# Performance work log

Measured on AMD Instinct MI355X. Metric: run time of the kernel, lower is better.

The kernel has to match this reference:

```python
import jax, jax.numpy as jnp
import numpy as np

B, L, D = 2, 2048, 2048
N, K, H = 16, 8, 128
EPS = 1e-6
ROPE_THETA = 1000000
K_MASK = -2.3819763e+38


def rms_norm(x, w, eps=EPS):
    dtype = x.dtype
    rms = jnp.sqrt(jnp.mean(x.astype(jnp.float32) ** 2, axis=-1, keepdims=True) + eps)
    return (w * x / rms).astype(dtype)


def apply_rope(inputs, positions, head_dim, rope_theta=ROPE_THETA):
    # inputs: [B, L, n, H], positions: [B, L]
    fraction = 2 * jnp.arange(0, head_dim // 2, dtype=jnp.float32) / head_dim
    timescale = rope_theta ** fraction  # [H/2]
    sinusoid = positions[..., jnp.newaxis] / timescale[jnp.newaxis, jnp.newaxis, :]  # [B,L,H/2]
    sinusoid = sinusoid[..., jnp.newaxis, :]  # [B,L,1,H/2]
    sin, cos = jnp.sin(sinusoid), jnp.cos(sinusoid)
    first, second = jnp.split(inputs, 2, axis=-1)
    out = jnp.concatenate([first * cos - second * sin, second * cos + first * sin], axis=-1)
    return out.astype(inputs.dtype)


def setup_inputs() -> dict:
    key = jax.random.key(0)
    ks = jax.random.split(key, 6)
    x = jax.random.normal(ks[0], (B, L, D), dtype=jnp.float32)
    position_ids = jnp.broadcast_to(jnp.arange(L, dtype=jnp.int32)[None, :], (B, L))
    # causal mask [B, L, S]
    attn_mask = jnp.broadcast_to(jnp.tril(jnp.ones((L, L), dtype=bool))[None], (B, L, L))
    wq = jax.random.normal(ks[1], (D, N, H), dtype=jnp.float32) * 0.02
    wk = jax.random.normal(ks[2], (D, K, H), dtype=jnp.float32) * 0.02
    wv = jax.random.normal(ks[3], (D, K, H), dtype=jnp.float32) * 0.02
    wo = jax.random.normal(ks[4], (N, H, D), dtype=jnp.float32) * 0.02
    q_norm_w = jnp.ones((H,), dtype=jnp.float32)
    k_norm_w = jnp.ones((H,), dtype=jnp.float32)
    return {"x": x, "position_ids": position_ids, "attn_mask": attn_mask,
            "wq": wq, "wk": wk, "wv": wv, "wo": wo,
            "q_norm_w": q_norm_w, "k_norm_w": k_norm_w}


def reference(x, position_ids, attn_mask, wq, wk, wv, wo, q_norm_w, k_norm_w):
    scale = H ** (-0.5)
    q = jnp.einsum('BLD,DNH->BLNH', x, wq)  # [B,L,N,H]
    k = jnp.einsum('BSD,DKH->BSKH', x, wk)  # [B,S,K,H]
    v = jnp.einsum('BSD,DKH->BSKH', x, wv)
    q = rms_norm(q, q_norm_w)
    k = rms_norm(k, k_norm_w)
    q = apply_rope(q, position_ids, H)
    k = apply_rope(k, position_ids, H)
    b, l, n, h = q.shape
    s = k.shape[1]
    kk = k.shape[2]
    q = q.reshape((b, l, kk, n // kk, h))
    attn = jnp.einsum('BLKGH,BSKH->BKGLS', q, k) * scale
    attn = attn.reshape((b, n, l, s))
    attn = jnp.where(jnp.expand_dims(attn_mask, -3), attn, K_MASK)
    attn = jax.nn.softmax(attn.astype(jnp.float32), axis=-1).astype(k.dtype)
    attn = attn.reshape((b, kk, n // kk, l, s))
    qkv = jnp.einsum('BKGLS,BSKH->BLKGH', attn, v).reshape((b, l, n, h))
    out = jnp.einsum('BLNH,NHD->BLD', qkv, wo)
    return out
```

## Files before the change

### kernel.cpp

```cpp
#include <hip/hip_runtime.h>

#define B_ 2
#define L_ 2048
#define D_ 2048
#define NH_ 16
#define KH_ 8
#define HD_ 128

typedef __attribute__((ext_vector_type(8))) short short8;
typedef __attribute__((ext_vector_type(4))) short short4v;
typedef __attribute__((ext_vector_type(4))) float floatx4;

__device__ __forceinline__ unsigned short f2bf(float f) {
  unsigned u = __float_as_uint(f);
  unsigned r = (u + 0x7fffu + ((u >> 16) & 1u)) >> 16;
  return (unsigned short)r;
}
__device__ __forceinline__ float bf2f(unsigned short h) {
  return __uint_as_float(((unsigned)h) << 16);
}
__device__ __forceinline__ void gl_lds16(const void* g, void* l) {
  __builtin_amdgcn_global_load_lds(
      (const __attribute__((address_space(1))) unsigned int*)g,
      (__attribute__((address_space(3))) unsigned int*)l, 16, 0, 0);
}

__global__ __launch_bounds__(256) void cvt_f32_bf16(const float* __restrict__ in,
                                                    unsigned short* __restrict__ out) {
  long i = ((long)blockIdx.x * 256 + threadIdx.x) * 4;
  float4 v = *(const float4*)(in + i);
  ushort4 o;
  o.x = f2bf(v.x); o.y = f2bf(v.y); o.z = f2bf(v.z); o.w = f2bf(v.w);
  *(ushort4*)(out + i) = o;
}

__global__ __launch_bounds__(256) void transpose_all(const float* __restrict__ wq,
                                                     const float* __restrict__ wk,
                                                     const float* __restrict__ wv,
                                                     const float* __restrict__ wo,
                                                     unsigned short* __restrict__ wqkv_t,
                                                     unsigned short* __restrict__ wo_t) {
  __shared__ float tile[32][33];
  int id = blockIdx.x;
  const float* in;
  unsigned short* out;
  int C, sh;
  if (id < 4096) {
    in = wq; out = wqkv_t; C = 2048; sh = 6;
  } else if (id < 6144) {
    in = wk; out = wqkv_t + 2048L * 2048; C = 1024; sh = 5; id -= 4096;
  } else if (id < 8192) {
    in = wv; out = wqkv_t + 3072L * 2048; C = 1024; sh = 5; id -= 6144;
  } else {
    in = wo; out = wo_t; C = 2048; sh = 6; id -= 8192;
  }
  int c0 = (id & ((1 << sh) - 1)) * 32, r0 = (id >> sh) * 32;
  int tx = threadIdx.x, ty = threadIdx.y;
#pragma unroll
  for (int i = 0; i < 4; i++)
    tile[ty + i * 8][tx] = in[(long)(r0 + ty + i * 8) * C + c0 + tx];
  __syncthreads();
#pragma unroll
  for (int i = 0; i < 4; i++) {
    int oc = ty + i * 8;
    out[(long)(c0 + oc) * 2048 + r0 + tx] = f2bf(tile[tx][oc]);
  }
}

__global__ __launch_bounds__(256) void transpose_v(const unsigned short* __restrict__ qkv,
                                                   unsigned short* __restrict__ vT) {
  __shared__ unsigned short tile[32][33];
  int l0 = blockIdx.x * 32, h0 = blockIdx.y * 32;
  int bk = blockIdx.z;
  int b = bk >> 3, kh = bk & 7;
  int tx = threadIdx.x, ty = threadIdx.y;
  const unsigned short* src = qkv + (long)b * L_ * 4096 + 3072 + kh * 128;
#pragma unroll
  for (int i = 0; i < 4; i++)
    tile[ty + i * 8][tx] = src[(long)(l0 + ty + i * 8) * 4096 + h0 + tx];
  __syncthreads();
  unsigned short* dst = vT + (long)bk * HD_ * L_;
#pragma unroll
  for (int i = 0; i < 4; i++)
    dst[(long)(h0 + ty + i * 8) * L_ + l0 + tx] = tile[tx][ty + i * 8];
}

template <int OUT_BF16>
__global__ __launch_bounds__(256, 3) void gemm128(const unsigned short* __restrict__ A,
                                                  const unsigned short* __restrict__ Bt,
                                                  void* __restrict__ C,
                                                  int M, int N, int K) {
  __shared__ unsigned short As[128 * 64];
  __shared__ unsigned short Bs[128 * 64];
  const int t = threadIdx.x;
  const int lane = t & 63, w = t >> 6;
  const int wy = w >> 1, wx = w & 1;
  const int col = lane & 15, quad = lane >> 4;
  const long m0 = (long)blockIdx.y * 128, n0 = (long)blockIdx.x * 128;
  floatx4 acc[4][4];
#pragma unroll
  for (int i = 0; i < 4; i++)
#pragma unroll
    for (int j = 0; j < 4; j++) acc[i][j] = (floatx4)0.0f;
  const int rs = t >> 3, bs = t & 7;
  for (int kt = 0; kt < K; kt += 64) {
#pragma unroll
    for (int i = 0; i < 4; i++) {
      int r = i * 32 + rs;
      gl_lds16(A + (m0 + r) * (long)K + kt + ((bs ^ (r & 7)) << 3),
               &As[(i * 32 + w * 8) * 64]);
      gl_lds16(Bt + (n0 + r) * (long)K + kt + ((bs ^ (r & 7)) << 3),
               &Bs[(i * 32 + w * 8) * 64]);
    }
    __syncthreads();
#pragma unroll
    for (int ks = 0; ks < 2; ks++) {
      short8 af[4], bf[4];
#pragma unroll
      for (int mi = 0; mi < 4; mi++) {
        int row = wy * 64 + mi * 16 + col;
        int blk = ks * 4 + quad;
        af[mi] = *(const short8*)&As[row * 64 + ((blk ^ (row & 7)) << 3)];
      }
#pragma unroll
      for (int ni = 0; ni < 4; ni++) {
        int row = wx * 64 + ni * 16 + col;
        int blk = ks * 4 + quad;
        bf[ni] = *(const short8*)&Bs[row * 64 + ((blk ^ (row & 7)) << 3)];
      }
#pragma unroll
      for (int mi = 0; mi < 4; mi++)
#pragma unroll
        for (int ni = 0; ni < 4; ni++)
          acc[mi][ni] = __builtin_amdgcn_mfma_f32_16x16x32_bf16(af[mi], bf[ni],
                                                                acc[mi][ni], 0, 0, 0);
    }
    __syncthreads();
  }
#pragma unroll
  for (int mi = 0; mi < 4; mi++)
#pragma unroll
    for (int r = 0; r < 4; r++) {
      long row = m0 + wy * 64 + mi * 16 + quad * 4 + r;
#pragma unroll
      for (int ni = 0; ni < 4; ni++) {
        long cg = n0 + wx * 64 + ni * 16 + col;
        float val = acc[mi][ni][r];
        if (OUT_BF16)
          ((unsigned short*)C)[row * N + cg] = f2bf(val);
        else
          ((float*)C)[row * N + cg] = val;
      }
    }
}

__global__ __launch_bounds__(256) void rmsrope(const unsigned short* __restrict__ qkv,
                                               const int* __restrict__ pos,
                                               const float* __restrict__ qw,
                                               const float* __restrict__ kw,
                                               unsigned short* __restrict__ qo,
                                               unsigned short* __restrict__ ko) {
  const int t = threadIdx.x, lane = t & 63, w = t >> 6;
  const int gid = blockIdx.x * 4 + w;
  const int row = gid / 24;
  const int hd = gid - row * 24;
  const int b = row >> 11, l = row & 2047;
  const unsigned short* src = qkv + (long)row * 4096 + hd * 128;
  float x0 = bf2f(src[lane]);
  float x1 = bf2f(src[lane + 64]);
  float ss = x0 * x0 + x1 * x1;
#pragma unroll
  for (int off = 32; off; off >>= 1) ss += __shfl_xor(ss, off);
  float inv = 1.0f / sqrtf(ss * (1.0f / 128.0f) + 1e-6f);
  const float* nw = (hd < 16) ? qw : kw;
  x0 = nw[lane] * x0 * inv;
  x1 = nw[lane + 64] * x1 * inv;
  float p = (float)pos[row];
  float ang = p * exp2f((float)lane * -0.31143075889f);
  float s, c;
  sincosf(ang, &s, &c);
  float o0 = x0 * c - x1 * s;
  float o1 = x1 * c + x0 * s;
  unsigned short* dst;
  if (hd < 16) {
    const float QSC = 0.08838834764831845f * 1.4426950408889634f;
    o0 *= QSC;
    o1 *= QSC;
    dst = qo + (((long)b * NH_ + hd) * L_ + l) * HD_;
  } else {
    dst = ko + (((long)b * KH_ + (hd - 16)) * L_ + l) * HD_;
  }
  dst[lane] = f2bf(o0);
  dst[lane + 64] = f2bf(o1);
}

__global__ __launch_bounds__(256, 2) void flash(const unsigned short* __restrict__ Q,
                                                const unsigned short* __restrict__ Kg,
                                                const unsigned short* __restrict__ VT,
                                                unsigned short* __restrict__ Og) {
  __shared__ unsigned short Ks[64 * 128];
  __shared__ unsigned short Vs[128 * 64];
  const int n = blockIdx.y, b = blockIdx.z;
  const int qt = b ? (15 - blockIdx.x) : blockIdx.x;
  const int t = threadIdx.x, lane = t & 63, w = t >> 6;
  const int col = lane & 15, quad = lane >> 4;
  const int kvh = n >> 1;
  const unsigned short* kb = Kg + ((long)b * KH_ + kvh) * L_ * HD_;
  const unsigned short* vtb = VT + ((long)b * KH_ + kvh) * HD_ * L_;
  const int l0 = qt * 128;
  const int steps = 2 * qt + 2;
  const unsigned short* qb = Q + (((long)b * NH_ + n) * L_ + l0) * HD_;

  short8 qf[2][4];
#pragma unroll
  for (int mi = 0; mi < 2; mi++)
#pragma unroll
    for (int ks = 0; ks < 4; ks++)
      qf[mi][ks] = *(const short8*)(qb + (w * 32 + mi * 16 + col) * 128 + ks * 32 + quad * 8);

  floatx4 o[2][8];
#pragma unroll
  for (int mi = 0; mi < 2; mi++)
#pragma unroll
    for (int nf = 0; nf < 8; nf++) o[mi][nf] = (floatx4)0.0f;
  float lrow[2] = {0.0f, 0.0f};

  for (int st = 0; st < steps; st++) {
    const int s0 = st * 64;
    {
      const int rK = t >> 4, blkK = t & 15;
#pragma unroll
      for (int i = 0; i < 4; i++) {
        int r = i * 16 + rK;
        int gblk = (blkK & 8) | ((blkK ^ r) & 7);
        gl_lds16(kb + (long)(s0 + r) * 128 + gblk * 8, &Ks[(i * 16 + w * 4) * 128]);
      }
    }
    {
      const int rV = t >> 3, blkV = t & 7;
#pragma unroll
      for (int j = 0; j < 4; j++) {
        int r = j * 32 + rV;
        int gblk = (blkV ^ r) & 7;
        gl_lds16(vtb + (long)r * L_ + s0 + gblk * 8, &Vs[(j * 32 + w * 8) * 64]);
      }
    }
    __syncthreads();

    floatx4 sa[2][4];
#pragma unroll
    for (int mi = 0; mi < 2; mi++)
#pragma unroll
      for (int sf = 0; sf < 4; sf++) sa[mi][sf] = (floatx4)0.0f;
#pragma unroll
    for (int ks = 0; ks < 4; ks++) {
      short8 bf[4];
#pragma unroll
      for (int sf = 0; sf < 4; sf++) {
        int srow = sf * 16 + col;
        int blk = ks * 4 + quad;
        bf[sf] = *(const short8*)&Ks[srow * 128 + (((blk & 8) | ((blk ^ srow) & 7)) << 3)];
      }
#pragma unroll
      for (int mi = 0; mi < 2; mi++)
#pragma unroll
        for (int sf = 0; sf < 4; sf++)
          sa[mi][sf] = __builtin_amdgcn_mfma_f32_16x16x32_bf16(bf[sf], qf[mi][ks],
                                                               sa[mi][sf], 0, 0, 0);
    }

    if (st >= steps - 2) {
#pragma unroll
      for (int mi = 0; mi < 2; mi++) {
        int lg = l0 + w * 32 + mi * 16 + col;
#pragma unroll
        for (int sf = 0; sf < 4; sf++)
#pragma unroll
          for (int r = 0; r < 4; r++) {
            int sg = s0 + sf * 16 + quad * 4 + r;
            if (sg > lg) sa[mi][sf][r] = -3.0e38f;
          }
      }
    }

    short4v pb[2][4];
#pragma unroll
    for (int mi = 0; mi < 2; mi++)
#pragma unroll
      for (int sf = 0; sf < 4; sf++) {
#pragma unroll
        for (int r = 0; r < 4; r++) {
          float pv = exp2f(sa[mi][sf][r] - 17.0f);
          lrow[mi] += pv;
          pb[mi][sf][r] = (short)f2bf(pv);
        }
      }

#pragma unroll
    for (int ks = 0; ks < 4; ks++) {
#pragma unroll
      for (int nf = 0; nf < 8; nf++) {
        int h = nf * 16 + col;
        int soff = ks * 16 + quad * 4;
        int blk = soff >> 3;
        short4v va = *(const short4v*)&Vs[h * 64 + ((blk ^ (h & 7)) << 3) + (soff & 7)];
#pragma unroll
        for (int mi = 0; mi < 2; mi++)
          o[mi][nf] = __builtin_amdgcn_mfma_f32_16x16x16bf16_1k(va, pb[mi][ks],
                                                                o[mi][nf], 0, 0, 0);
      }
    }
    __syncthreads();
  }

#pragma unroll
  for (int mi = 0; mi < 2; mi++) {
    float s = lrow[mi];
    s += __shfl_xor(s, 16);
    s += __shfl_xor(s, 32);
    float inv = 1.0f / s;
    int lg = l0 + w * 32 + mi * 16 + col;
    unsigned short* dst = Og + (((long)b * L_ + lg) * NH_ + n) * HD_;
#pragma unroll
    for (int nf = 0; nf < 8; nf++) {
      ushort4 ov;
      ov.x = f2bf(o[mi][nf][0] * inv);
      ov.y = f2bf(o[mi][nf][1] * inv);
      ov.z = f2bf(o[mi][nf][2] * inv);
      ov.w = f2bf(o[mi][nf][3] * inv);
      *(ushort4*)(dst + nf * 16 + quad * 4) = ov;
    }
  }
}

extern "C" void kernel_launch(void* const* d_in, const int* in_sizes, int n_in,
                              void* d_out, int out_size, void* d_ws, size_t ws_size,
                              hipStream_t stream) {
  const float* x = (const float*)d_in[0];
  const int* pos = (const int*)d_in[1];
  const float* wq = (const float*)d_in[3];
  const float* wk = (const float*)d_in[4];
  const float* wv = (const float*)d_in[5];
  const float* wo = (const float*)d_in[6];
  const float* qnw = (const float*)d_in[7];
  const float* knw = (const float*)d_in[8];
  float* out = (float*)d_out;

  char* ws = (char*)d_ws;
  unsigned short* xb     = (unsigned short*)(ws + 0);
  unsigned short* wqkv_t = (unsigned short*)(ws + 16777216);
  unsigned short* wo_t   = (unsigned short*)(ws + 33554432);
  unsigned short* qkv    = (unsigned short*)(ws + 41943040);
  unsigned short* q      = (unsigned short*)(ws + 75497472);
  unsigned short* k      = (unsigned short*)(ws + 92274688);
  unsigned short* vT     = (unsigned short*)(ws + 100663296);
  unsigned short* ao     = (unsigned short*)(ws + 109051904);
  if (ws_size < 125829120) return;

  cvt_f32_bf16<<<8192, 256, 0, stream>>>(x, xb);
  dim3 tb(32, 8);
  transpose_all<<<12288, tb, 0, stream>>>(wq, wk, wv, wo, wqkv_t, wo_t);
  gemm128<1><<<dim3(32, 32), 256, 0, stream>>>(xb, wqkv_t, qkv, 4096, 4096, 2048);
  rmsrope<<<24576, 256, 0, stream>>>(qkv, pos, qnw, knw, q, k);
  transpose_v<<<dim3(64, 4, 16), tb, 0, stream>>>(qkv, vT);
  flash<<<dim3(16, NH_, B_), 256, 0, stream>>>(q, k, vT, ao);
  gemm128<0><<<dim3(16, 32), 256, 0, stream>>>(ao, wo_t, out, 4096, 2048, 2048);
}
```

Baseline: 362.8 us.

## Merge prep kernels, split-K output GEMM, and restage P through LDS in flash

Fuses the x conversion and weight transposes into one launch, and fuses RMS-norm/RoPE with the V transpose into another, cutting launch count. The output projection GEMM is split along K into two halves that accumulate into a zeroed output with atomic adds, doubling the grid to improve occupancy. The flash kernel now writes P to LDS and re-reads it so the PV product can use the wider 16x16x32 MFMA with 8-element fragments. This costs an extra LDS buffer and more LDS traffic. The flash epilogue now stores output with scalar per-element writes instead of vector stores.

```diff
diff --git a/kernel.cpp b/kernel.cpp
--- a/kernel.cpp
+++ b/kernel.cpp
@@ -25,23 +25,26 @@
       (__attribute__((address_space(3))) unsigned int*)l, 16, 0, 0);
 }
 
-__global__ __launch_bounds__(256) void cvt_f32_bf16(const float* __restrict__ in,
-                                                    unsigned short* __restrict__ out) {
-  long i = ((long)blockIdx.x * 256 + threadIdx.x) * 4;
-  float4 v = *(const float4*)(in + i);
-  ushort4 o;
-  o.x = f2bf(v.x); o.y = f2bf(v.y); o.z = f2bf(v.z); o.w = f2bf(v.w);
-  *(ushort4*)(out + i) = o;
-}
-
-__global__ __launch_bounds__(256) void transpose_all(const float* __restrict__ wq,
-                                                     const float* __restrict__ wk,
-                                                     const float* __restrict__ wv,
-                                                     const float* __restrict__ wo,
-                                                     unsigned short* __restrict__ wqkv_t,
-                                                     unsigned short* __restrict__ wo_t) {
+__global__ __launch_bounds__(256) void prep1(const float* __restrict__ x,
+                                             const float* __restrict__ wq,
+                                             const float* __restrict__ wk,
+                                             const float* __restrict__ wv,
+                                             const float* __restrict__ wo,
+                                             unsigned short* __restrict__ xb,
+                                             unsigned short* __restrict__ wqkv_t,
+                                             unsigned short* __restrict__ wo_t) {
+  int id = blockIdx.x;
+  int t = threadIdx.x;
+  if (id < 8192) {
+    long i = ((long)id * 256 + t) * 4;
+    float4 v = *(const float4*)(x + i);
+    ushort4 o;
+    o.x = f2bf(v.x); o.y = f2bf(v.y); o.z = f2bf(v.z); o.w = f2bf(v.w);
+    *(ushort4*)(xb + i) = o;
+    return;
+  }
+  id -= 8192;
   __shared__ float tile[32][33];
-  int id = blockIdx.x;
   const float* in;
   unsigned short* out;
   int C, sh;
@@ -55,7 +58,7 @@
     in = wo; out = wo_t; C = 2048; sh = 6; id -= 8192;
   }
   int c0 = (id & ((1 << sh) - 1)) * 32, r0 = (id >> sh) * 32;
-  int tx = threadIdx.x, ty = threadIdx.y;
+  int tx = t & 31, ty = t >> 5;
 #pragma unroll
   for (int i = 0; i < 4; i++)
     tile[ty + i * 8][tx] = in[(long)(r0 + ty + i * 8) * C + c0 + tx];
@@ -67,13 +70,56 @@
   }
 }
 
-__global__ __launch_bounds__(256) void transpose_v(const unsigned short* __restrict__ qkv,
-                                                   unsigned short* __restrict__ vT) {
+__global__ __launch_bounds__(256) void prep2(const unsigned short* __restrict__ qkv,
+                                             const int* __restrict__ pos,
+                                             const float* __restrict__ qw,
+                                             const float* __restrict__ kw,
+                                             unsigned short* __restrict__ qo,
+                                             unsigned short* __restrict__ ko,
+                                             unsigned short* __restrict__ vT) {
+  int id = blockIdx.x;
+  int t = threadIdx.x;
+  if (id < 24576) {
+    const int lane = t & 63, w = t >> 6;
+    const int gid = id * 4 + w;
+    const int row = gid / 24;
+    const int hd = gid - row * 24;
+    const int b = row >> 11, l = row & 2047;
+    const unsigned short* src = qkv + (long)row * 4096 + hd * 128;
+    float x0 = bf2f(src[lane]);
+    float x1 = bf2f(src[lane + 64]);
+    float ss = x0 * x0 + x1 * x1;
+#pragma unroll
+    for (int off = 32; off; off >>= 1) ss += __shfl_xor(ss, off);
+    float inv = 1.0f / sqrtf(ss * (1.0f / 128.0f) + 1e-6f);
+    const float* nw = (hd < 16) ? qw : kw;
+    x0 = nw[lane] * x0 * inv;
+    x1 = nw[lane + 64] * x1 * inv;
+    float p = (float)pos[row];
+    float ang = p * exp2f((float)lane * -0.31143075889f);
+    float s, c;
+    sincosf(ang, &s, &c);
+    float o0 = x0 * c - x1 * s;
+    float o1 = x1 * c + x0 * s;
+    unsigned short* dst;
+    if (hd < 16) {
+      const float QSC = 0.08838834764831845f * 1.4426950408889634f;
+      o0 *= QSC;
+      o1 *= QSC;
+      dst = qo + (((long)b * NH_ + hd) * L_ + l) * HD_;
+    } else {
+      dst = ko + (((long)b * KH_ + (hd - 16)) * L_ + l) * HD_;
+    }
+    dst[lane] = f2bf(o0);
+    dst[lane + 64] = f2bf(o1);
+    return;
+  }
+  id -= 24576;
   __shared__ unsigned short tile[32][33];
-  int l0 = blockIdx.x * 32, h0 = blockIdx.y * 32;
-  int bk = blockIdx.z;
+  int l0 = (id & 63) * 32, h0 = ((id >> 6) & 3) * 32;
+  int bk = id >> 8;
   int b = bk >> 3, kh = bk & 7;
-  int tx = threadIdx.x, ty = threadIdx.y;
+  int tx = t & 31, ty = t >> 5;
   const unsigned short* src = qkv + (long)b * L_ * 4096 + 3072 + kh * 128;
 #pragma unroll
   for (int i = 0; i < 4; i++)
@@ -85,7 +131,7 @@
     dst[(long)(h0 + ty + i * 8) * L_ + l0 + tx] = tile[tx][ty + i * 8];
 }
 
-template <int OUT_BF16>
+template <int MODE>
 __global__ __launch_bounds__(256, 3) void gemm128(const unsigned short* __restrict__ A,
                                                   const unsigned short* __restrict__ Bt,
                                                   void* __restrict__ C,
@@ -97,13 +143,15 @@
   const int wy = w >> 1, wx = w & 1;
   const int col = lane & 15, quad = lane >> 4;
   const long m0 = (long)blockIdx.y * 128, n0 = (long)blockIdx.x * 128;
+  const int kbeg = (MODE == 2) ? blockIdx.z * (K >> 1) : 0;
+  const int kend = (MODE == 2) ? kbeg + (K >> 1) : K;
   floatx4 acc[4][4];
 #pragma unroll
   for (int i = 0; i < 4; i++)
 #pragma unroll
     for (int j = 0; j < 4; j++) acc[i][j] = (floatx4)0.0f;
   const int rs = t >> 3, bs = t & 7;
-  for (int kt = 0; kt < K; kt += 64) {
+  for (int kt = kbeg; kt < kend; kt += 64) {
 #pragma unroll
     for (int i = 0; i < 4; i++) {
       int r = i * 32 + rs;
@@ -146,52 +194,12 @@
       for (int ni = 0; ni < 4; ni++) {
         long cg = n0 + wx * 64 + ni * 16 + col;
         float val = acc[mi][ni][r];
-        if (OUT_BF16)
+        if (MODE == 1)
           ((unsigned short*)C)[row * N + cg] = f2bf(val);
         else
-          ((float*)C)[row * N + cg] = val;
-      }
-    }
-}
-
-__global__ __launch_bounds__(256) void rmsrope(const unsigned short* __restrict__ qkv,
-                                               const int* __restrict__ pos,
-                                               const float* __restrict__ qw,
-                                               const float* __restrict__ kw,
-                                               unsigned short* __restrict__ qo,
-                                               unsigned short* __restrict__ ko) {
-  const int t = threadIdx.x, lane = t & 63, w = t >> 6;
-  const int gid = blockIdx.x * 4 + w;
-  const int row = gid / 24;
-  const int hd = gid - row * 24;
-  const int b = row >> 11, l = row & 2047;
-  const unsigned short* src = qkv + (long)row * 4096 + hd * 128;
-  float x0 = bf2f(src[lane]);
-  float x1 = bf2f(src[lane + 64]);
-  float ss = x0 * x0 + x1 * x1;
-#pragma unroll
-  for (int off = 32; off; off >>= 1) ss += __shfl_xor(ss, off);
-  float inv = 1.0f / sqrtf(ss * (1.0f / 128.0f) + 1e-6f);
-  const float* nw = (hd < 16) ? qw : kw;
-  x0 = nw[lane] * x0 * inv;
-  x1 = nw[lane + 64] * x1 * inv;
-  float p = (float)pos[row];
-  float ang = p * exp2f((float)lane * -0.31143075889f);
-  float s, c;
-  sincosf(ang, &s, &c);
-  float o0 = x0 * c - x1 * s;
-  float o1 = x1 * c + x0 * s;
-  unsigned short* dst;
-  if (hd < 16) {
-    const float QSC = 0.08838834764831845f * 1.4426950408889634f;
-    o0 *= QSC;
-    o1 *= QSC;
-    dst = qo + (((long)b * NH_ + hd) * L_ + l) * HD_;
-  } else {
-    dst = ko + (((long)b * KH_ + (hd - 16)) * L_ + l) * HD_;
-  }
-  dst[lane] = f2bf(o0);
-  dst[lane + 64] = f2bf(o1);
+          unsafeAtomicAdd(&((float*)C)[row * N + cg], val);
+      }
+    }
 }
 
 __global__ __launch_bounds__(256, 2) void flash(const unsigned short* __restrict__ Q,
@@ -200,6 +208,7 @@
                                                 unsigned short* __restrict__ Og) {
   __shared__ unsigned short Ks[64 * 128];
   __shared__ unsigned short Vs[128 * 64];
+  __shared__ unsigned short Ps[128 * 72];
   const int n = blockIdx.y, b = blockIdx.z;
   const int qt = b ? (15 - blockIdx.x) : blockIdx.x;
   const int t = threadIdx.x, lane = t & 63, w = t >> 6;
@@ -283,32 +292,39 @@
       }
     }
 
-    short4v pb[2][4];
 #pragma unroll
     for (int mi = 0; mi < 2; mi++)
 #pragma unroll
       for (int sf = 0; sf < 4; sf++) {
+        short4v pk;
 #pragma unroll
         for (int r = 0; r < 4; r++) {
           float pv = exp2f(sa[mi][sf][r] - 17.0f);
           lrow[mi] += pv;
-          pb[mi][sf][r] = (short)f2bf(pv);
+          pk[r] = (short)f2bf(pv);
         }
-      }
-
-#pragma unroll
-    for (int ks = 0; ks < 4; ks++) {
+        *(short4v*)&Ps[(w * 32 + mi * 16 + col) * 72 + sf * 16 + quad * 4] = pk;
+      }
+
+#pragma unroll
+    for (int ks = 0; ks < 2; ks++) {
+      short8 pf[2];
+#pragma unroll
+      for (int mi = 0; mi < 2; mi++)
+        pf[mi] = *(const short8*)&Ps[(w * 32 + mi * 16 + col) * 72 + ks * 32 + quad * 8];
+      short8 vf[8];
 #pragma unroll
       for (int nf = 0; nf < 8; nf++) {
         int h = nf * 16 + col;
-        int soff = ks * 16 + quad * 4;
-        int blk = soff >> 3;
-        short4v va = *(const short4v*)&Vs[h * 64 + ((blk ^ (h & 7)) << 3) + (soff & 7)];
-#pragma unroll
-        for (int mi = 0; mi < 2; mi++)
-          o[mi][nf] = __builtin_amdgcn_mfma_f32_16x16x16bf16_1k(va, pb[mi][ks],
-                                                                o[mi][nf], 0, 0, 0);
-      }
+        int blk = ks * 4 + quad;
+        vf[nf] = *(const short8*)&Vs[h * 64 + ((blk ^ (h & 7)) << 3)];
+      }
+#pragma unroll
+      for (int mi = 0; mi < 2; mi++)
+#pragma unroll
+        for (int nf = 0; nf < 8; nf++)
+          o[mi][nf] = __builtin_amdgcn_mfma_f32_16x16x32_bf16(pf[mi], vf[nf],
+                                                              o[mi][nf], 0, 0, 0);
     }
     __syncthreads();
   }
@@ -318,17 +334,14 @@
     float s = lrow[mi];
     s += __shfl_xor(s, 16);
     s += __shfl_xor(s, 32);
-    float inv = 1.0f / s;
-    int lg = l0 + w * 32 + mi * 16 + col;
-    unsigned short* dst = Og + (((long)b * L_ + lg) * NH_ + n) * HD_;
-#pragma unroll
-    for (int nf = 0; nf < 8; nf++) {
-      ushort4 ov;
-      ov.x = f2bf(o[mi][nf][0] * inv);
-      ov.y = f2bf(o[mi][nf][1] * inv);
-      ov.z = f2bf(o[mi][nf][2] * inv);
-      ov.w = f2bf(o[mi][nf][3] * inv);
-      *(ushort4*)(dst + nf * 16 + quad * 4) = ov;
+#pragma unroll
+    for (int r = 0; r < 4; r++) {
+      float inv = 1.0f / __shfl(s, quad * 4 + r);
+      int lg = l0 + w * 32 + mi * 16 + quad * 4 + r;
+      unsigned short* dst = Og + (((long)b * L_ + lg) * NH_ + n) * HD_;
+#pragma unroll
+      for (int nf = 0; nf < 8; nf++)
+        dst[nf * 16 + col] = f2bf(o[mi][nf][r] * inv);
     }
   }
 }
@@ -357,12 +370,10 @@
   unsigned short* ao     = (unsigned short*)(ws + 109051904);
   if (ws_size < 125829120) return;
 
-  cvt_f32_bf16<<<8192, 256, 0, stream>>>(x, xb);
-  dim3 tb(32, 8);
-  transpose_all<<<12288, tb, 0, stream>>>(wq, wk, wv, wo, wqkv_t, wo_t);
+  hipMemsetAsync(d_out, 0, (size_t)out_size * 4, stream);
+  prep1<<<20480, 256, 0, stream>>>(x, wq, wk, wv, wo, xb, wqkv_t, wo_t);
   gemm128<1><<<dim3(32, 32), 256, 0, stream>>>(xb, wqkv_t, qkv, 4096, 4096, 2048);
-  rmsrope<<<24576, 256, 0, stream>>>(qkv, pos, qnw, knw, q, k);
-  transpose_v<<<dim3(64, 4, 16), tb, 0, stream>>>(qkv, vT);
+  prep2<<<28672, 256, 0, stream>>>(qkv, pos, qnw, knw, q, k, vT);
   flash<<<dim3(16, NH_, B_), 256, 0, stream>>>(q, k, vT, ao);
-  gemm128<0><<<dim3(16, 32), 256, 0, stream>>>(ao, wo_t, out, 4096, 2048, 2048);
-}
+  gemm128<2><<<dim3(16, 32, 2), 256, 0, stream>>>(ao, wo_t, out, 4096, 2048, 2048);
+}
```

Measured after the change: 382.6 us. 1.05x slower.
